# Kernel optimization log

Measured on AMD Instinct MI355X. Metric: run time of the kernel, lower is better.

## Reference

```python
import jax, jax.numpy as jnp
import numpy as np

N_TOKENS = 16384
D_IN = 1024
D_HID = 4096
D_OUT = 1024
N_EXPERTS = 8


def setup_inputs() -> dict:
    key = jax.random.key(0)
    ks = jax.random.split(key, 7)
    s_in = 1.0 / np.sqrt(D_IN)
    s_hid = 1.0 / np.sqrt(D_HID)
    return {
        "x": jax.random.normal(ks[0], (N_TOKENS, D_IN), dtype=jnp.float32),
        "Wr": jax.random.uniform(ks[1], (D_IN, N_EXPERTS), jnp.float32, -s_in, s_in),
        "br": jax.random.uniform(ks[2], (N_EXPERTS,), jnp.float32, -s_in, s_in),
        "W1": jax.random.uniform(ks[3], (N_EXPERTS, D_IN, D_HID), jnp.float32, -s_in, s_in),
        "b1": jax.random.uniform(ks[4], (N_EXPERTS, D_HID), jnp.float32, -s_in, s_in),
        "W2": jax.random.uniform(ks[5], (N_EXPERTS, D_HID, D_OUT), jnp.float32, -s_hid, s_hid),
        "b2": jax.random.uniform(ks[6], (N_EXPERTS, D_OUT), jnp.float32, -s_hid, s_hid),
    }


def reference(x, Wr, br, W1, b1, W2, b2):
    # Router: softmax over expert logits, hard top-1 dispatch (argmax).
    # Note: output is NOT scaled by routing probs in the original module.
    logits = x @ Wr + br                      # [N, E]
    expert_idx = jnp.argmax(logits, axis=-1)  # [N] (argmax of softmax == argmax of logits)

    n_experts = W1.shape[0]
    out = jnp.zeros((x.shape[0], W2.shape[-1]), dtype=x.dtype)
    # world_size=1 -> all_to_all is identity; masked per-expert dense FFN + combine.
    # Fixed small loop over experts (structurally distinct weights), vectorized over tokens.
    for e in range(n_experts):
        mask = (expert_idx == e)[:, None]                 # [N, 1]
        xe = jnp.where(mask, x, 0.0)                      # zero out tokens not routed here
        y = jax.nn.relu(xe @ W1[e] + b1[e]) @ W2[e] + b2[e]  # [N, D_OUT]
        out = jnp.where(mask, y, out)
    return out
```

## Files before the change

### kernel.cpp

```cpp
#include <hip/hip_runtime.h>
#include <cstdint>

#define NT   16384
#define DIN  1024
#define DHID 4096
#define DOUT 1024
#define NE   8
#define NMT  136

typedef unsigned short u16;
typedef short bf16x8 __attribute__((ext_vector_type(8)));
typedef float f32x4  __attribute__((ext_vector_type(4)));

__device__ __forceinline__ u16 f2b(float f) {
  union { float f; unsigned u; } a; a.f = f;
  unsigned u = a.u;
  return (u16)((u + 0x7FFFu + ((u >> 16) & 1u)) >> 16);
}

__device__ __forceinline__ void gl_lds16(const u16* g, u16* l) {
  __builtin_amdgcn_global_load_lds(
      (const __attribute__((address_space(1))) void*)g,
      (__attribute__((address_space(3))) void*)l,
      16, 0, 0);
}

__global__ void router_kernel(const float* __restrict__ x, const float* __restrict__ Wr,
                              const float* __restrict__ br, u16* __restrict__ Xb,
                              int* __restrict__ eidx, int* __restrict__ counts) {
  int t = blockIdx.x * 4 + (threadIdx.x >> 6);
  int lane = threadIdx.x & 63;
  const float* xr = x + (size_t)t * DIN;
  u16* xbr = Xb + (size_t)t * DIN;
  float acc[NE];
#pragma unroll
  for (int e = 0; e < NE; e++) acc[e] = 0.f;
#pragma unroll
  for (int i = 0; i < DIN / 64; i++) {
    int k = lane + i * 64;
    float xv = xr[k];
    xbr[k] = f2b(xv);
    const float4 w0 = *(const float4*)(Wr + (size_t)k * NE);
    const float4 w1 = *(const float4*)(Wr + (size_t)k * NE + 4);
    acc[0] += xv * w0.x; acc[1] += xv * w0.y; acc[2] += xv * w0.z; acc[3] += xv * w0.w;
    acc[4] += xv * w1.x; acc[5] += xv * w1.y; acc[6] += xv * w1.z; acc[7] += xv * w1.w;
  }
#pragma unroll
  for (int off = 32; off > 0; off >>= 1) {
#pragma unroll
    for (int e = 0; e < NE; e++) acc[e] += __shfl_down(acc[e], off, 64);
  }
  if (lane == 0) {
    int best = 0; float bv = acc[0] + br[0];
#pragma unroll
    for (int e = 1; e < NE; e++) {
      float v = acc[e] + br[e];
      if (v > bv) { bv = v; best = e; }
    }
    eidx[t] = best;
    atomicAdd(&counts[best], 1);
  }
}

__global__ void zero_kernel(int* __restrict__ p) {
  if (threadIdx.x < 16) p[threadIdx.x] = 0;
}

__global__ void scan_kernel(const int* __restrict__ counts, int* __restrict__ offsets,
                            int4* __restrict__ tiles) {
  if (threadIdx.x == 0) {
    int s = 0, nt = 0;
    for (int e = 0; e < NE; e++) {
      int c = counts[e];
      offsets[e] = s;
      for (int m0 = 0; m0 < c; m0 += 128) {
        int v = c - m0; if (v > 128) v = 128;
        tiles[nt++] = make_int4(e, s + m0, v, 0);
      }
      s += c;
    }
    offsets[NE] = s;
    while (nt < NMT) tiles[nt++] = make_int4(0, 0, 0, 0);
  }
}

__global__ void scatter_kernel(const int* __restrict__ eidx, const int* __restrict__ offsets,
                               int* __restrict__ cursor, int* __restrict__ perm) {
  int t = blockIdx.x * blockDim.x + threadIdx.x;
  if (t >= NT) return;
  int e = eidx[t];
  int pos = offsets[e] + atomicAdd(&cursor[e], 1);
  perm[pos] = t;
}

__global__ void transpose_cvt_kernel(const float* __restrict__ W, u16* __restrict__ Wt,
                                     int K, int H) {
  __shared__ float tile[64][65];
  const int e = blockIdx.z;
  const int k0 = blockIdx.x * 64, h0 = blockIdx.y * 64;
  const float* src = W + (size_t)e * K * H;
  u16* dst = Wt + (size_t)e * K * H;
  const int tid = threadIdx.x;
#pragma unroll
  for (int i = 0; i < 4; i++) {
    int idx = tid + i * 256;
    int r = idx >> 4;
    int c = (idx & 15) * 4;
    const float4 v = *(const float4*)(src + (size_t)(k0 + r) * H + h0 + c);
    tile[r][c] = v.x; tile[r][c + 1] = v.y; tile[r][c + 2] = v.z; tile[r][c + 3] = v.w;
  }
  __syncthreads();
#pragma unroll
  for (int i = 0; i < 4; i++) {
    int idx = tid + i * 256;
    int r = idx >> 4;
    int c = (idx & 15) * 4;
    ushort4 o;
    o.x = f2b(tile[c][r]); o.y = f2b(tile[c + 1][r]);
    o.z = f2b(tile[c + 2][r]); o.w = f2b(tile[c + 3][r]);
    *(ushort4*)(dst + (size_t)(h0 + r) * K + k0 + c) = o;
  }
}

template<bool GATHER_A, bool STORE_HIDDEN>
__global__ __launch_bounds__(256) void moe_gemm(
    const u16* __restrict__ A, const u16* __restrict__ Bt,
    const float* __restrict__ bias,
    const int* __restrict__ perm, const int4* __restrict__ tiles,
    u16* __restrict__ Hout, float* __restrict__ Fout,
    int K, int N) {
  const int4 ti = tiles[blockIdx.y];
  const int valid = ti.z;
  if (valid == 0) return;
  const int e = ti.x;
  const int base_p = ti.y;
  const int n0 = blockIdx.x * 128;

  __shared__ u16 sA[2 * 128 * 32];
  __shared__ u16 sB[2 * 128 * 32];

  const int tid = threadIdx.x;
  const int lane = tid & 63;
  const int wave = tid >> 6;
  const int wm = (wave >> 1) * 64;
  const int wn = (wave & 1) * 64;
  const int quad = lane >> 4;
  const int l15 = lane & 15;

  const int rr = lane >> 2;
  const int cb = (lane & 3) * 8;

  const int rA0 = wave * 16 + rr;
  const int rA1 = rA0 + 64;

  int pa0 = base_p + rA0; if (pa0 > NT - 1) pa0 = NT - 1;
  int pa1 = base_p + rA1; if (pa1 > NT - 1) pa1 = NT - 1;
  const int arow0 = GATHER_A ? perm[pa0] : pa0;
  const int arow1 = GATHER_A ? perm[pa1] : pa1;
  const u16* aptr0 = A + (size_t)arow0 * K + cb;
  const u16* aptr1 = A + (size_t)arow1 * K + cb;
  const u16* bptr0 = Bt + ((size_t)e * N + n0 + rA0) * K + cb;
  const u16* bptr1 = Bt + ((size_t)e * N + n0 + rA1) * K + cb;

  u16* dA0 = &sA[wave * 512];
  u16* dA1 = &sA[wave * 512 + 2048];
  u16* dB0 = &sB[wave * 512];
  u16* dB1 = &sB[wave * 512 + 2048];

  f32x4 acc[4][4];
#pragma unroll
  for (int mi = 0; mi < 4; mi++)
#pragma unroll
    for (int ni = 0; ni < 4; ni++)
      acc[mi][ni] = (f32x4){0.f, 0.f, 0.f, 0.f};

  const int kiters = K >> 6;
  for (int kt = 0; kt < kiters; kt++) {
    if (kt) __syncthreads();
    gl_lds16(aptr0,      dA0);
    gl_lds16(aptr1,      dA1);
    gl_lds16(bptr0,      dB0);
    gl_lds16(bptr1,      dB1);
    gl_lds16(aptr0 + 32, dA0 + 4096);
    gl_lds16(aptr1 + 32, dA1 + 4096);
    gl_lds16(bptr0 + 32, dB0 + 4096);
    gl_lds16(bptr1 + 32, dB1 + 4096);
    aptr0 += 64; aptr1 += 64; bptr0 += 64; bptr1 += 64;
    __syncthreads();

#pragma unroll
    for (int h = 0; h < 2; h++) {
      bf16x8 af[4], bfr[4];
#pragma unroll
      for (int mi = 0; mi < 4; mi++)
        af[mi] = *(const bf16x8*)&sA[h * 4096 + (wm + mi * 16 + l15) * 32 + quad * 8];
#pragma unroll
      for (int ni = 0; ni < 4; ni++)
        bfr[ni] = *(const bf16x8*)&sB[h * 4096 + (wn + ni * 16 + l15) * 32 + quad * 8];
#pragma unroll
      for (int mi = 0; mi < 4; mi++)
#pragma unroll
        for (int ni = 0; ni < 4; ni++)
          acc[mi][ni] = __builtin_amdgcn_mfma_f32_16x16x32_bf16(af[mi], bfr[ni], acc[mi][ni], 0, 0, 0);
    }
  }

  float bv[4];
#pragma unroll
  for (int ni = 0; ni < 4; ni++)
    bv[ni] = bias[(size_t)e * N + n0 + wn + ni * 16 + l15];

#pragma unroll
  for (int mi = 0; mi < 4; mi++) {
#pragma unroll
    for (int r = 0; r < 4; r++) {
      const int ml = wm + mi * 16 + quad * 4 + r;
      if (ml >= valid) continue;
      const int pp = base_p + ml;
      if (STORE_HIDDEN) {
        u16* orow = Hout + (size_t)pp * N + n0 + wn;
#pragma unroll
        for (int ni = 0; ni < 4; ni++) {
          float v = acc[mi][ni][r] + bv[ni];
          v = v > 0.f ? v : 0.f;
          orow[ni * 16 + l15] = f2b(v);
        }
      } else {
        const int token = perm[pp];
        float* orow = Fout + (size_t)token * N + n0 + wn;
#pragma unroll
        for (int ni = 0; ni < 4; ni++)
          orow[ni * 16 + l15] = acc[mi][ni][r] + bv[ni];
      }
    }
  }
}

__global__ void sentinel_kernel(float* __restrict__ out, int n) {
  int i = blockIdx.x * blockDim.x + threadIdx.x;
  if (i < n) out[i] = 31337.0f;
}

extern "C" void kernel_launch(void* const* d_in, const int* in_sizes, int n_in,
                              void* d_out, int out_size, void* d_ws, size_t ws_size,
                              hipStream_t stream) {
  const float* x  = (const float*)d_in[0];
  const float* Wr = (const float*)d_in[1];
  const float* br = (const float*)d_in[2];
  const float* W1 = (const float*)d_in[3];
  const float* b1 = (const float*)d_in[4];
  const float* W2 = (const float*)d_in[5];
  const float* b2 = (const float*)d_in[6];
  float* out = (float*)d_out;

  const size_t szXb  = (size_t)NT * DIN * 2;
  const size_t szW1t = (size_t)NE * DIN * DHID * 2;
  const size_t szW2t = (size_t)NE * DHID * DOUT * 2;
  const size_t szHid = (size_t)NT * DHID * 2;
  char* ws = (char*)d_ws;
  u16* Xb   = (u16*)ws;
  u16* W1t  = (u16*)(ws + szXb);
  u16* W2t  = (u16*)(ws + szXb + szW1t);
  u16* Hid  = (u16*)(ws + szXb + szW1t + szW2t);
  int* perm = (int*)(ws + szXb + szW1t + szW2t + szHid);
  int* eidx = perm + NT;
  int* ctrl = eidx + NT;
  int* counts  = ctrl;
  int* cursor  = ctrl + 8;
  int* offsets = ctrl + 16;
  int4* tiles  = (int4*)(ctrl + 32);
  const size_t NEED = szXb + szW1t + szW2t + szHid + (size_t)NT * 4 * 2 + 4096;

  if (ws_size < NEED) {
    sentinel_kernel<<<(out_size + 255) / 256, 256, 0, stream>>>(out, out_size);
    return;
  }

  zero_kernel<<<1, 64, 0, stream>>>(ctrl);
  transpose_cvt_kernel<<<dim3(DIN / 64, DHID / 64, NE), 256, 0, stream>>>(W1, W1t, DIN, DHID);
  transpose_cvt_kernel<<<dim3(DHID / 64, DOUT / 64, NE), 256, 0, stream>>>(W2, W2t, DHID, DOUT);
  router_kernel<<<NT / 4, 256, 0, stream>>>(x, Wr, br, Xb, eidx, counts);
  scan_kernel<<<1, 64, 0, stream>>>(counts, offsets, tiles);
  scatter_kernel<<<NT / 256, 256, 0, stream>>>(eidx, offsets, cursor, perm);

  moe_gemm<true, true><<<dim3(DHID / 128, NMT), 256, 0, stream>>>(
      Xb, W1t, b1, perm, tiles, Hid, nullptr, DIN, DHID);
  moe_gemm<false, false><<<dim3(DOUT / 128, NMT), 256, 0, stream>>>(
      Hid, W2t, b2, perm, tiles, nullptr, out, DHID, DOUT);
}
```

Baseline: 1.012 ms.

## Use 256x256 eight-phase pipelined GEMM for first MoE layer

```diff
diff --git a/kernel.cpp b/kernel.cpp
--- a/kernel.cpp
+++ b/kernel.cpp
@@ -7,6 +7,7 @@
 #define DOUT 1024
 #define NE   8
 #define NMT  136
+#define NMT2 72
 
 typedef unsigned short u16;
 typedef short bf16x8 __attribute__((ext_vector_type(8)));
@@ -25,25 +26,45 @@
       16, 0, 0);
 }
 
+__device__ __forceinline__ void barrier_raw() {
+  asm volatile("" ::: "memory");
+  __builtin_amdgcn_s_barrier();
+  asm volatile("" ::: "memory");
+}
+__device__ __forceinline__ void lgkm0() {
+  asm volatile("s_waitcnt lgkmcnt(0)" ::: "memory");
+  __builtin_amdgcn_sched_barrier(0);
+}
+__device__ __forceinline__ void vm6() {
+  asm volatile("s_waitcnt vmcnt(6)" ::: "memory");
+}
+
 __global__ void router_kernel(const float* __restrict__ x, const float* __restrict__ Wr,
                               const float* __restrict__ br, u16* __restrict__ Xb,
                               int* __restrict__ eidx, int* __restrict__ counts) {
   int t = blockIdx.x * 4 + (threadIdx.x >> 6);
   int lane = threadIdx.x & 63;
-  const float* xr = x + (size_t)t * DIN;
-  u16* xbr = Xb + (size_t)t * DIN;
+  const float4* xr = (const float4*)(x + (size_t)t * DIN);
+  ushort4* xbr = (ushort4*)(Xb + (size_t)t * DIN);
   float acc[NE];
 #pragma unroll
   for (int e = 0; e < NE; e++) acc[e] = 0.f;
 #pragma unroll
-  for (int i = 0; i < DIN / 64; i++) {
-    int k = lane + i * 64;
-    float xv = xr[k];
-    xbr[k] = f2b(xv);
-    const float4 w0 = *(const float4*)(Wr + (size_t)k * NE);
-    const float4 w1 = *(const float4*)(Wr + (size_t)k * NE + 4);
-    acc[0] += xv * w0.x; acc[1] += xv * w0.y; acc[2] += xv * w0.z; acc[3] += xv * w0.w;
-    acc[4] += xv * w1.x; acc[5] += xv * w1.y; acc[6] += xv * w1.z; acc[7] += xv * w1.w;
+  for (int i = 0; i < DIN / 256; i++) {
+    int q = lane + i * 64;
+    float4 xv = xr[q];
+    ushort4 o;
+    o.x = f2b(xv.x); o.y = f2b(xv.y); o.z = f2b(xv.z); o.w = f2b(xv.w);
+    xbr[q] = o;
+    const float* wp = Wr + (size_t)q * 4 * NE;
+#pragma unroll
+    for (int kk = 0; kk < 4; kk++) {
+      float xs = (&xv.x)[kk];
+      const float4 w0 = *(const float4*)(wp + kk * NE);
+      const float4 w1 = *(const float4*)(wp + kk * NE + 4);
+      acc[0] += xs * w0.x; acc[1] += xs * w0.y; acc[2] += xs * w0.z; acc[3] += xs * w0.w;
+      acc[4] += xs * w1.x; acc[5] += xs * w1.y; acc[6] += xs * w1.z; acc[7] += xs * w1.w;
+    }
   }
 #pragma unroll
   for (int off = 32; off > 0; off >>= 1) {
@@ -67,9 +88,9 @@
 }
 
 __global__ void scan_kernel(const int* __restrict__ counts, int* __restrict__ offsets,
-                            int4* __restrict__ tiles) {
+                            int4* __restrict__ tiles, int4* __restrict__ tiles2) {
   if (threadIdx.x == 0) {
-    int s = 0, nt = 0;
+    int s = 0, nt = 0, nt2 = 0;
     for (int e = 0; e < NE; e++) {
       int c = counts[e];
       offsets[e] = s;
@@ -77,10 +98,15 @@
         int v = c - m0; if (v > 128) v = 128;
         tiles[nt++] = make_int4(e, s + m0, v, 0);
       }
+      for (int m0 = 0; m0 < c; m0 += 256) {
+        int v = c - m0; if (v > 256) v = 256;
+        tiles2[nt2++] = make_int4(e, s + m0, v, 0);
+      }
       s += c;
     }
     offsets[NE] = s;
     while (nt < NMT) tiles[nt++] = make_int4(0, 0, 0, 0);
+    while (nt2 < NMT2) tiles2[nt2++] = make_int4(0, 0, 0, 0);
   }
 }
 
@@ -93,13 +119,23 @@
   perm[pos] = t;
 }
 
-__global__ void transpose_cvt_kernel(const float* __restrict__ W, u16* __restrict__ Wt,
-                                     int K, int H) {
+__global__ void transpose_cvt_all(const float* __restrict__ W1, const float* __restrict__ W2,
+                                  u16* __restrict__ W1t, u16* __restrict__ W2t) {
   __shared__ float tile[64][65];
-  const int e = blockIdx.z;
-  const int k0 = blockIdx.x * 64, h0 = blockIdx.y * 64;
-  const float* src = W + (size_t)e * K * H;
-  u16* dst = Wt + (size_t)e * K * H;
+  int bid = blockIdx.x;
+  const float* src; u16* dst; int K, H, k0, h0;
+  if (bid < NE * 16 * 64) {
+    int e = bid >> 10, rem = bid & 1023;
+    K = DIN; H = DHID;
+    k0 = (rem & 15) * 64; h0 = (rem >> 4) * 64;
+    src = W1 + (size_t)e * DIN * DHID; dst = W1t + (size_t)e * DIN * DHID;
+  } else {
+    bid -= NE * 16 * 64;
+    int e = bid >> 10, rem = bid & 1023;
+    K = DHID; H = DOUT;
+    k0 = (rem >> 4) * 64; h0 = (rem & 15) * 64;
+    src = W2 + (size_t)e * DHID * DOUT; dst = W2t + (size_t)e * DHID * DOUT;
+  }
   const int tid = threadIdx.x;
 #pragma unroll
   for (int i = 0; i < 4; i++) {
@@ -234,6 +270,171 @@
       }
     }
   }
+}
+
+#define RXA0 0
+#define RXA1 8192
+#define RXB0 16384
+#define RXB1 24576
+#define RYA0 32768
+#define RYA1 40960
+#define RYB0 49152
+#define RYB1 57344
+
+__global__ __launch_bounds__(512, 2) void moe_gemm1_8ph(
+    const u16* __restrict__ A, const u16* __restrict__ Bt,
+    const float* __restrict__ bias, const int* __restrict__ perm,
+    const int4* __restrict__ tiles, u16* __restrict__ Hout) {
+  const int4 ti = tiles[blockIdx.y];
+  const int valid = ti.z;
+  if (valid == 0) return;
+  const int e = ti.x;
+  const int base_p = ti.y;
+  const int n0 = blockIdx.x * 256;
+
+  __shared__ u16 lds[65536];
+
+  const int tid = threadIdx.x;
+  const int lane = tid & 63;
+  const int w = tid >> 6;
+  const int wr = w >> 2;
+  const int wc = w & 3;
+  const int quad = lane >> 4;
+  const int l15 = lane & 15;
+
+  const int srow = tid >> 3;
+  const int klog = ((tid & 7) << 3) ^ ((srow & 7) << 3);
+  int p0 = base_p + srow;        if (p0 > NT - 1) p0 = NT - 1;
+  int p1 = base_p + 64 + srow;   if (p1 > NT - 1) p1 = NT - 1;
+  int p2 = base_p + 128 + srow;  if (p2 > NT - 1) p2 = NT - 1;
+  int p3 = base_p + 192 + srow;  if (p3 > NT - 1) p3 = NT - 1;
+  const u16* pA00 = A + (size_t)perm[p0] * DIN + klog;
+  const u16* pA01 = A + (size_t)perm[p1] * DIN + klog;
+  const u16* pA10 = A + (size_t)perm[p2] * DIN + klog;
+  const u16* pA11 = A + (size_t)perm[p3] * DIN + klog;
+  const u16* pB00 = Bt + ((size_t)e * DHID + n0 + srow)       * DIN + klog;
+  const u16* pB01 = Bt + ((size_t)e * DHID + n0 + 64 + srow)  * DIN + klog;
+  const u16* pB10 = Bt + ((size_t)e * DHID + n0 + 128 + srow) * DIN + klog;
+  const u16* pB11 = Bt + ((size_t)e * DHID + n0 + 192 + srow) * DIN + klog;
+
+#define STG(RB, P0, P1, KO) \
+  do { gl_lds16((P0) + (KO), &lds[(RB) + w * 512]); \
+       gl_lds16((P1) + (KO), &lds[(RB) + 4096 + w * 512]); } while (0)
+
+  STG(RXA0, pA00, pA01, 0);
+  STG(RXA1, pA10, pA11, 0);
+  STG(RXB0, pB00, pB01, 0);
+  STG(RXB1, pB10, pB11, 0);
+  STG(RYB0, pB00, pB01, 64);
+  STG(RYB1, pB10, pB11, 64);
+  STG(RYA0, pA00, pA01, 64);
+  vm6();
+  barrier_raw();
+
+  const int aX = RXA0 + wr * 8192;
+  const int bX = RXB0 + (wc >> 1) * 8192;
+  const int aY = RYA0 + wr * 8192;
+  const int bY = RYB0 + (wc >> 1) * 8192;
+  const int swz = (l15 & 7) << 3;
+  const int brow = (wc & 1) * 64 + l15;
+
+  bf16x8 aF[4][2], bF[4][2];
+  f32x4 acc[8][4];
+#pragma unroll
+  for (int i = 0; i < 8; i++)
+#pragma unroll
+    for (int j2 = 0; j2 < 4; j2++) acc[i][j2] = (f32x4){0.f, 0.f, 0.f, 0.f};
+
+#define RDA(BASE, MH) do { _Pragma("unroll") \
+  for (int mi = 0; mi < 4; mi++) { _Pragma("unroll") \
+    for (int h = 0; h < 2; h++) \
+      aF[mi][h] = *(const bf16x8*)&lds[(BASE) + ((MH) * 64 + mi * 16 + l15) * 64 + \
+                                       ((h * 32 + quad * 8) ^ swz)]; } } while (0)
+
+#define RDB(BASE) do { _Pragma("unroll") \
+  for (int ni = 0; ni < 4; ni++) { _Pragma("unroll") \
+    for (int h = 0; h < 2; h++) \
+      bF[ni][h] = *(const bf16x8*)&lds[(BASE) + (brow + ni * 16) * 64 + \
+                                       ((h * 32 + quad * 8) ^ swz)]; } } while (0)
+
+#define MM(MH, NB) do { __builtin_amdgcn_s_setprio(1); _Pragma("unroll") \
+  for (int mi = 0; mi < 4; mi++) { _Pragma("unroll") \
+    for (int ni = 0; ni < 2; ni++) { _Pragma("unroll") \
+      for (int h = 0; h < 2; h++) \
+        acc[(MH) * 4 + mi][(NB) + ni] = __builtin_amdgcn_mfma_f32_16x16x32_bf16( \
+            aF[mi][h], bF[(NB) + ni][h], acc[(MH) * 4 + mi][(NB) + ni], 0, 0, 0); } } \
+  __builtin_amdgcn_s_setprio(0); } while (0)
+
+  const int NITER = DIN / 128;
+  for (int j = 0; j < NITER; j++) {
+    const int ky1 = (2 * j + 1) * 64;
+    int t2 = 2 * j + 2; if (t2 > 15) t2 = 15;
+    int t3 = 2 * j + 3; if (t3 > 15) t3 = 15;
+    const int kx = t2 * 64, ky2 = t3 * 64;
+    RDA(aX, 0); RDB(bX);
+    STG(RYA1, pA10, pA11, ky1);
+    barrier_raw(); lgkm0();
+    MM(0, 0);
+    barrier_raw();
+    STG(RXB0, pB00, pB01, kx);
+    barrier_raw(); lgkm0();
+    MM(0, 2);
+    barrier_raw();
+    RDA(aX, 1);
+    STG(RXB1, pB10, pB11, kx);
+    barrier_raw(); lgkm0();
+    MM(1, 2);
+    barrier_raw();
+    STG(RXA0, pA00, pA01, kx);
+    barrier_raw(); lgkm0();
+    MM(1, 0);
+    vm6();
+    barrier_raw();
+    RDA(aY, 0); RDB(bY);
+    STG(RXA1, pA10, pA11, kx);
+    barrier_raw(); lgkm0();
+    MM(0, 0);
+    barrier_raw();
+    STG(RYB0, pB00, pB01, ky2);
+    barrier_raw(); lgkm0();
+    MM(0, 2);
+    barrier_raw();
+    RDA(aY, 1);
+    STG(RYB1, pB10, pB11, ky2);
+    barrier_raw(); lgkm0();
+    MM(1, 2);
+    barrier_raw();
+    STG(RYA0, pA00, pA01, ky2);
+    barrier_raw(); lgkm0();
+    MM(1, 0);
+    vm6();
+    barrier_raw();
+  }
+
+  const int col0 = n0 + wc * 64;
+  float bv[4];
+#pragma unroll
+  for (int ni = 0; ni < 4; ni++)
+    bv[ni] = bias[(size_t)e * DHID + col0 + ni * 16 + l15];
+#pragma unroll
+  for (int mi8 = 0; mi8 < 8; mi8++) {
+#pragma unroll
+    for (int r = 0; r < 4; r++) {
+      const int ml = wr * 128 + mi8 * 16 + quad * 4 + r;
+      if (ml >= valid) continue;
+      u16* orow = Hout + (size_t)(base_p + ml) * DHID + col0;
+#pragma unroll
+      for (int ni = 0; ni < 4; ni++) {
+        float v = acc[mi8][ni][r] + bv[ni];
+        v = v > 0.f ? v : 0.f;
+        orow[ni * 16 + l15] = f2b(v);
+      }
+    }
+  }
+#undef STG
+#undef RDA
+#undef RDB
+#undef MM
 }
 
 __global__ void sentinel_kernel(float* __restrict__ out, int n) {
@@ -268,7 +469,8 @@
   int* counts  = ctrl;
   int* cursor  = ctrl + 8;
   int* offsets = ctrl + 16;
-  int4* tiles  = (int4*)(ctrl + 32);
+  int4* tiles   = (int4*)(ctrl + 32);
+  int4* tiles2  = tiles + NMT;
   const size_t NEED = szXb + szW1t + szW2t + szHid + (size_t)NT * 4 * 2 + 4096;
 
   if (ws_size < NEED) {
@@ -277,14 +479,13 @@
   }
 
   zero_kernel<<<1, 64, 0, stream>>>(ctrl);
-  transpose_cvt_kernel<<<dim3(DIN / 64, DHID / 64, NE), 256, 0, stream>>>(W1, W1t, DIN, DHID);
-  transpose_cvt_kernel<<<dim3(DHID / 64, DOUT / 64, NE), 256, 0, stream>>>(W2, W2t, DHID, DOUT);
+  transpose_cvt_all<<<NE * 16 * 64 * 2, 256, 0, stream>>>(W1, W2, W1t, W2t);
   router_kernel<<<NT / 4, 256, 0, stream>>>(x, Wr, br, Xb, eidx, counts);
-  scan_kernel<<<1, 64, 0, stream>>>(counts, offsets, tiles);
+  scan_kernel<<<1, 64, 0, stream>>>(counts, offsets, tiles, tiles2);
   scatter_kernel<<<NT / 256, 256, 0, stream>>>(eidx, offsets, cursor, perm);
 
-  moe_gemm<true, true><<<dim3(DHID / 128, NMT), 256, 0, stream>>>(
-      Xb, W1t, b1, perm, tiles, Hid, nullptr, DIN, DHID);
+  moe_gemm1_8ph<<<dim3(DHID / 256, NMT2), 512, 0, stream>>>(
+      Xb, W1t, b1, perm, tiles2, Hid);
   moe_gemm<false, false><<<dim3(DOUT / 128, NMT), 256, 0, stream>>>(
       Hid, W2t, b2, perm, tiles, nullptr, out, DHID, DOUT);
 }
```

Result: no change. 1.016 ms (+0.4%).
